# Kernel tuning notes

Hardware: AMD Instinct MI355X
Metric: run time of the kernel (lower is better)

## Reference

```python
import jax, jax.numpy as jnp
import numpy as np

N_NODES = 50000
N_EDGES = 800000
D_FEAT = 64
UNITS = 128  # concat=True -> each kernel maps D_FEAT -> UNITS//2


def setup_inputs() -> dict:
    key = jax.random.key(0)
    k1, k2, k3, k4, k5 = jax.random.split(key, 5)
    x = jax.random.normal(k1, (N_NODES, D_FEAT), dtype=jnp.float32)
    edge_index = jax.random.randint(k2, (2, N_EDGES), 0, N_NODES, dtype=jnp.int64)
    edge_weight = jax.random.uniform(k3, (N_EDGES,), dtype=jnp.float32)
    glorot = np.sqrt(6.0 / (D_FEAT + UNITS // 2)).astype(np.float32)
    self_kernel = jax.random.uniform(k4, (D_FEAT, UNITS // 2), dtype=jnp.float32, minval=-glorot, maxval=glorot)
    neighbor_kernel = jax.random.uniform(k5, (D_FEAT, UNITS // 2), dtype=jnp.float32, minval=-glorot, maxval=glorot)
    bias = jnp.zeros((UNITS,), dtype=jnp.float32)
    return {"x": x, "edge_index": edge_index, "edge_weight": edge_weight,
            "self_kernel": self_kernel, "neighbor_kernel": neighbor_kernel, "bias": bias}


def reference(x, edge_index, edge_weight, self_kernel, neighbor_kernel, bias):
    num_nodes = x.shape[0]
    row, col = edge_index[0], edge_index[1]  # row: target node, col: source neighbor
    # gather neighbor features and apply edge weights
    neighbor_x = x[col] * edge_weight[:, None]  # [E, D]
    # segment-mean over incoming edges of each target node
    sums = jax.ops.segment_sum(neighbor_x, row, num_segments=num_nodes)  # [N, D]
    counts = jax.ops.segment_sum(jnp.ones_like(edge_weight), row, num_segments=num_nodes)  # [N]
    neighbor_mean = sums / jnp.maximum(counts, 1.0)[:, None]
    # dual projection + concat (concat=True)
    from_self = x @ self_kernel              # [N, UNITS//2]
    from_neigh = neighbor_mean @ neighbor_kernel  # [N, UNITS//2]
    h = jnp.concatenate([from_self, from_neigh], axis=1) + bias
    h = jax.nn.relu(h)
    # normalize=False -> no l2 normalize
    return h
```

## Files before the change

### kernel.cpp

```cpp
#include <hip/hip_runtime.h>


typedef unsigned long long ull;
typedef __attribute__((ext_vector_type(8))) short bf16x8;
typedef __attribute__((ext_vector_type(4))) float f32x4;

constexpr int N_NODES = 50000;
constexpr int N_EDGES = 800000;
constexpr int D = 64;
constexpr int UNITS = 128;
constexpr int NB = (N_NODES + 255) / 256;
constexpr int SC_EPT = 16;
constexpr int SC_THREADS = 256;
constexpr int SC_CHUNK = SC_EPT * SC_THREADS;
constexpr int SC_BLOCKS = (N_EDGES + SC_CHUNK - 1) / SC_CHUNK;
constexpr int NS_EPT = 24;
constexpr int PREP_BLOCKS = 2048;
constexpr int NTILES = N_NODES / 16;
constexpr int PJ_BLOCKS = (NTILES + 3) / 4;

__device__ __forceinline__ unsigned f2bf(float f) {
    unsigned u = __float_as_uint(f);
    return (u + 0x7fffu + ((u >> 16) & 1u)) >> 16;
}
__device__ __forceinline__ float bf2f(unsigned b) {
    return __uint_as_float(b << 16);
}

__global__ __launch_bounds__(256) void prep(const float* __restrict__ x,
                                            unsigned* __restrict__ xh,
                                            const int* __restrict__ ei,
                                            int* __restrict__ partial) {
    constexpr int XW = N_NODES * (D / 2);
    for (int i = blockIdx.x * 256 + threadIdx.x; i < XW; i += PREP_BLOCKS * 256) {
        const float2 v = ((const float2*)x)[i];
        xh[i] = f2bf(v.x) | (f2bf(v.y) << 16);
    }
    if (blockIdx.x < SC_BLOCKS) {
        __shared__ int lh[NB];
        for (int i = threadIdx.x; i < NB; i += 256) lh[i] = 0;
        __syncthreads();
        const int base4 = blockIdx.x * (SC_CHUNK / 4);
        #pragma unroll
        for (int j = 0; j < 4; ++j) {
            const int idx4 = base4 + threadIdx.x + j * 256;
            if (idx4 * 4 < N_EDGES) {
                const int4 r4 = ((const int4*)ei)[idx4];
                atomicAdd(&lh[r4.x >> 8], 1);
                atomicAdd(&lh[r4.y >> 8], 1);
                atomicAdd(&lh[r4.z >> 8], 1);
                atomicAdd(&lh[r4.w >> 8], 1);
            }
        }
        __syncthreads();
        int* row = partial + (size_t)blockIdx.x * NB;
        for (int i = threadIdx.x; i < NB; i += 256) row[i] = lh[i];
    }
}

__global__ __launch_bounds__(256) void scan_cols(int* __restrict__ partial,
                                                 int* __restrict__ btot) {
    __shared__ int s[256];
    const int b = blockIdx.x;
    const int t = threadIdx.x;
    const int v = (t < SC_BLOCKS) ? partial[(size_t)t * NB + b] : 0;
    s[t] = v;
    __syncthreads();
    for (int d2 = 1; d2 < 256; d2 <<= 1) {
        int u = (t >= d2) ? s[t - d2] : 0;
        __syncthreads();
        s[t] += u;
        __syncthreads();
    }
    if (t < SC_BLOCKS) partial[(size_t)t * NB + b] = s[t] - v;
    if (t == 255) btot[b] = s[255];
}

__global__ __launch_bounds__(SC_THREADS) void edge_scatter(const int* __restrict__ ei,
                                                           const float* __restrict__ ew,
                                                           const int* __restrict__ partial,
                                                           const int* __restrict__ btot,
                                                           ull* __restrict__ packed) {
    __shared__ int sb[256];
    __shared__ int lbase[NB];
    __shared__ int lcur[NB];
    const int t = threadIdx.x;
    const int bv = (t < NB) ? btot[t] : 0;
    sb[t] = bv;
    __syncthreads();
    for (int d2 = 1; d2 < 256; d2 <<= 1) {
        int u = (t >= d2) ? sb[t - d2] : 0;
        __syncthreads();
        sb[t] += u;
        __syncthreads();
    }
    const int* row = partial + (size_t)blockIdx.x * NB;
    if (t < NB) {
        lbase[t] = (sb[t] - bv) + row[t];
        lcur[t]  = 0;
    }
    __syncthreads();

    const int base4 = blockIdx.x * (SC_CHUNK / 4);
    int4   r4[4];
    int4   c4[4];
    float4 w4[4];
    #pragma unroll
    for (int j = 0; j < 4; ++j) {
        const int idx4 = base4 + t + j * 256;
        if (idx4 * 4 < N_EDGES) {
            r4[j] = ((const int4*)ei)[idx4];
            c4[j] = ((const int4*)(ei + N_EDGES))[idx4];
            w4[j] = ((const float4*)ew)[idx4];
        } else {
            r4[j] = make_int4(-1, -1, -1, -1);
            c4[j] = make_int4(0, 0, 0, 0);
            w4[j] = make_float4(0.f, 0.f, 0.f, 0.f);
        }
    }
    #pragma unroll
    for (int j = 0; j < 4; ++j) {
        const int   rr[4] = {r4[j].x, r4[j].y, r4[j].z, r4[j].w};
        const int   cc[4] = {c4[j].x, c4[j].y, c4[j].z, c4[j].w};
        const float ww[4] = {w4[j].x, w4[j].y, w4[j].z, w4[j].w};
        #pragma unroll
        for (int k = 0; k < 4; ++k) {
            const int r = rr[k];
            if (r >= 0) {
                const int bb   = r >> 8;
                const int lpos = atomicAdd(&lcur[bb], 1);
                const unsigned hi = (unsigned)cc[k] | ((unsigned)(r & 255) << 16);
                packed[lbase[bb] + lpos] = ((ull)hi << 32) | (ull)(unsigned)__float_as_uint(ww[k]);
            }
        }
    }
}

__global__ __launch_bounds__(256) void node_sort(const int* __restrict__ btot,
                                                 int* __restrict__ offs,
                                                 const ull* __restrict__ packed,
                                                 unsigned* __restrict__ cedges) {
    __shared__ int cur[256];
    __shared__ int sc[256];
    __shared__ int sBase, sEnd;
    const int b = blockIdx.x;
    const int t = threadIdx.x;

    const int bv = (t < NB) ? btot[t] : 0;
    sc[t] = bv;
    __syncthreads();
    for (int d2 = 1; d2 < 256; d2 <<= 1) {
        int u = (t >= d2) ? sc[t - d2] : 0;
        __syncthreads();
        sc[t] += u;
        __syncthreads();
    }
    if (t == b) { sBase = sc[t] - bv; sEnd = sc[t]; }
    __syncthreads();
    const int s = sBase;
    const int e = sEnd;

    ull st[NS_EPT];
    #pragma unroll
    for (int i = 0; i < NS_EPT; ++i) {
        const int idx = s + t + i * 256;
        st[i] = (idx < e) ? packed[idx] : ~0ull;
    }
    cur[t] = 0;
    __syncthreads();
    #pragma unroll
    for (int i = 0; i < NS_EPT; ++i) {
        if (st[i] != ~0ull) atomicAdd(&cur[(int)((st[i] >> 48) & 0xff)], 1);
    }
    __syncthreads();
    const int v = cur[t];
    sc[t] = v;
    __syncthreads();
    for (int d2 = 1; d2 < 256; d2 <<= 1) {
        int u = (t >= d2) ? sc[t - d2] : 0;
        __syncthreads();
        sc[t] += u;
        __syncthreads();
    }
    const int excl = sc[t] - v;
    const int n = b * 256 + t;
    if (n < N_NODES) offs[n] = s + excl;
    if (b == 0 && t == 0) offs[N_NODES] = N_EDGES;
    cur[t] = excl;
    __syncthreads();
    #pragma unroll
    for (int i = 0; i < NS_EPT; ++i) {
        if (st[i] != ~0ull) {
            const int r8  = (int)((st[i] >> 48) & 0xff);
            const int pos = atomicAdd(&cur[r8], 1);
            const unsigned hi  = (unsigned)(st[i] >> 32);
            const unsigned col = hi & 0xffffu;
            const unsigned wbf = f2bf(__uint_as_float((unsigned)st[i]));
            cedges[s + pos] = (col << 16) | wbf;
        }
    }
}

__global__ __launch_bounds__(256) void sage_aggregate(const unsigned* __restrict__ xh,
                                                      const int* __restrict__ offs,
                                                      const unsigned* __restrict__ cedges,
                                                      unsigned* __restrict__ meanh) {
    const int n = (blockIdx.x * 256 + threadIdx.x) >> 5;
    if (n >= N_NODES) return;
    const int l32 = threadIdx.x & 31;
    const int eg  = l32 >> 3;
    const int wq  = l32 & 7;
    const int s = offs[n];
    const int t = offs[n + 1];

    float ax0 = 0.f, ay0 = 0.f, ax1 = 0.f, ay1 = 0.f;
    float ax2 = 0.f, ay2 = 0.f, ax3 = 0.f, ay3 = 0.f;
    float bx0 = 0.f, by0 = 0.f, bx1 = 0.f, by1 = 0.f;
    float bx2 = 0.f, by2 = 0.f, bx3 = 0.f, by3 = 0.f;

    if (t > s) {
        const int tm1 = t - 1;
        for (int g = s; g < t; g += 8) {
            const int eA = g + eg;
            const int eB = g + 4 + eg;
            const unsigned cA = cedges[min(eA, tm1)];
            const unsigned cB = cedges[min(eB, tm1)];
            const float wA = (eA < t) ? bf2f(cA & 0xffffu) : 0.0f;
            const float wB = (eB < t) ? bf2f(cB & 0xffffu) : 0.0f;
            const uint4 vA = *(const uint4*)(xh + (size_t)(cA >> 16) * (D / 2) + wq * 4);
            const uint4 vB = *(const uint4*)(xh + (size_t)(cB >> 16) * (D / 2) + wq * 4);
            ax0 = fmaf(__uint_as_float(vA.x << 16),         wA, ax0);
            ay0 = fmaf(__uint_as_float(vA.x & 0xffff0000u), wA, ay0);
            ax1 = fmaf(__uint_as_float(vA.y << 16),         wA, ax1);
            ay1 = fmaf(__uint_as_float(vA.y & 0xffff0000u), wA, ay1);
            ax2 = fmaf(__uint_as_float(vA.z << 16),         wA, ax2);
            ay2 = fmaf(__uint_as_float(vA.z & 0xffff0000u), wA, ay2);
            ax3 = fmaf(__uint_as_float(vA.w << 16),         wA, ax3);
            ay3 = fmaf(__uint_as_float(vA.w & 0xffff0000u), wA, ay3);
            bx0 = fmaf(__uint_as_float(vB.x << 16),         wB, bx0);
            by0 = fmaf(__uint_as_float(vB.x & 0xffff0000u), wB, by0);
            bx1 = fmaf(__uint_as_float(vB.y << 16),         wB, bx1);
            by1 = fmaf(__uint_as_float(vB.y & 0xffff0000u), wB, by1);
            bx2 = fmaf(__uint_as_float(vB.z << 16),         wB, bx2);
            by2 = fmaf(__uint_as_float(vB.z & 0xffff0000u), wB, by2);
            bx3 = fmaf(__uint_as_float(vB.w << 16),         wB, bx3);
            by3 = fmaf(__uint_as_float(vB.w & 0xffff0000u), wB, by3);
        }
    }
    float sx0 = ax0 + bx0, sy0 = ay0 + by0;
    float sx1 = ax1 + bx1, sy1 = ay1 + by1;
    float sx2 = ax2 + bx2, sy2 = ay2 + by2;
    float sx3 = ax3 + bx3, sy3 = ay3 + by3;
    sx0 += __shfl_xor(sx0, 8);  sx0 += __shfl_xor(sx0, 16);
    sy0 += __shfl_xor(sy0, 8);  sy0 += __shfl_xor(sy0, 16);
    sx1 += __shfl_xor(sx1, 8);  sx1 += __shfl_xor(sx1, 16);
    sy1 += __shfl_xor(sy1, 8);  sy1 += __shfl_xor(sy1, 16);
    sx2 += __shfl_xor(sx2, 8);  sx2 += __shfl_xor(sx2, 16);
    sy2 += __shfl_xor(sy2, 8);  sy2 += __shfl_xor(sy2, 16);
    sx3 += __shfl_xor(sx3, 8);  sx3 += __shfl_xor(sx3, 16);
    sy3 += __shfl_xor(sy3, 8);  sy3 += __shfl_xor(sy3, 16);

    if (eg == 0) {
        const float inv = 1.0f / fmaxf((float)(t - s), 1.0f);
        uint4 r;
        r.x = f2bf(sx0 * inv) | (f2bf(sy0 * inv) << 16);
        r.y = f2bf(sx1 * inv) | (f2bf(sy1 * inv) << 16);
        r.z = f2bf(sx2 * inv) | (f2bf(sy2 * inv) << 16);
        r.w = f2bf(sx3 * inv) | (f2bf(sy3 * inv) << 16);
        *(uint4*)(meanh + (size_t)n * (D / 2) + wq * 4) = r;
    }
}

__global__ __launch_bounds__(256) void sage_project(const unsigned* __restrict__ xh,
                                                    const unsigned* __restrict__ meanh,
                                                    const float* __restrict__ skern,
                                                    const float* __restrict__ nkern,
                                                    const float* __restrict__ bias,
                                                    float* __restrict__ out) {
    const int lane = threadIdx.x & 63;
    const int wid  = (blockIdx.x * 256 + threadIdx.x) >> 6;
    const int r16  = lane & 15;
    const int g    = lane >> 4;

    bf16x8 bfrag[16];
    #pragma unroll
    for (int ct = 0; ct < 8; ++ct) {
        const float* K = (ct < 4) ? skern : nkern;
        const int col = (ct & 3) * 16 + r16;
        #pragma unroll
        for (int kh = 0; kh < 2; ++kh) {
            bf16x8 f;
            #pragma unroll
            for (int j = 0; j < 8; ++j) {
                const int k = kh * 32 + 8 * g + j;
                f[j] = (short)f2bf(K[k * 64 + col]);
            }
            bfrag[ct * 2 + kh] = f;
        }
    }

    if (wid >= NTILES) return;
    const int n0 = wid * 16;

    const unsigned* xrow = xh    + (size_t)(n0 + r16) * (D / 2);
    const unsigned* mrow = meanh + (size_t)(n0 + r16) * (D / 2);
    const bf16x8 aS0 = *(const bf16x8*)(xrow + 4 * g);
    const bf16x8 aS1 = *(const bf16x8*)(xrow + 16 + 4 * g);
    const bf16x8 aN0 = *(const bf16x8*)(mrow + 4 * g);
    const bf16x8 aN1 = *(const bf16x8*)(mrow + 16 + 4 * g);

    f32x4 acc[8];
    #pragma unroll
    for (int ct = 0; ct < 8; ++ct) {
        f32x4 c = {0.f, 0.f, 0.f, 0.f};
        c = __builtin_amdgcn_mfma_f32_16x16x32_bf16(ct < 4 ? aS0 : aN0, bfrag[ct * 2 + 0], c, 0, 0, 0);
        c = __builtin_amdgcn_mfma_f32_16x16x32_bf16(ct < 4 ? aS1 : aN1, bfrag[ct * 2 + 1], c, 0, 0, 0);
        acc[ct] = c;
    }

    #pragma unroll
    for (int ct = 0; ct < 8; ++ct) {
        const int col = (ct < 4 ? 0 : 64) + (ct & 3) * 16 + r16;
        const float bj = bias[col];
        #pragma unroll
        for (int r = 0; r < 4; ++r) {
            const int node = n0 + 4 * g + r;
            out[(size_t)node * UNITS + col] = fmaxf(acc[ct][r] + bj, 0.0f);
        }
    }
}

extern "C" void kernel_launch(void* const* d_in, const int* in_sizes, int n_in,
                              void* d_out, int out_size, void* d_ws, size_t ws_size,
                              hipStream_t stream) {
    const float* x     = (const float*)d_in[0];
    const int*   ei    = (const int*)  d_in[1];
    const float* ew    = (const float*)d_in[2];
    const float* skern = (const float*)d_in[3];
    const float* nkern = (const float*)d_in[4];
    const float* bias  = (const float*)d_in[5];
    float* out = (float*)d_out;

    auto align256 = [](size_t v) { return (v + 255) & ~size_t(255); };
    const size_t szM  = align256((size_t)SC_BLOCKS * NB * sizeof(int));
    const size_t szT  = align256((size_t)NB * sizeof(int));
    const size_t szNO = align256((size_t)(N_NODES + 1) * sizeof(int));
    const size_t szP  = align256((size_t)N_EDGES * sizeof(ull));
    const size_t szC  = align256((size_t)N_EDGES * sizeof(unsigned));
    const size_t szX  = align256((size_t)N_NODES * (D / 2) * sizeof(unsigned));

    char* w = (char*)d_ws;
    int*      partial = (int*)w;
    int*      btot    = (int*)(w + szM);
    int*      offs    = (int*)(w + szM + szT);
    ull*      packed  = (ull*)(w + szM + szT + szNO);
    unsigned* cedges  = (unsigned*)(w + szM + szT + szNO + szP);
    unsigned* xh      = (unsigned*)(w + szM + szT + szNO + szP + szC);
    unsigned* meanh   = (unsigned*)(w + szM + szT + szNO + szP + szC + szX);
    (void)ws_size; (void)in_sizes; (void)n_in; (void)out_size;

    prep          <<<PREP_BLOCKS, 256, 0, stream>>>(x, xh, ei, partial);
    scan_cols     <<<NB, 256, 0, stream>>>(partial, btot);
    edge_scatter  <<<SC_BLOCKS, SC_THREADS, 0, stream>>>(ei, ew, partial, btot, packed);
    node_sort     <<<NB, SC_THREADS, 0, stream>>>(btot, offs, packed, cedges);
    sage_aggregate<<<(N_NODES * 32 + 255) / 256, 256, 0, stream>>>(xh, offs, cedges, meanh);
    sage_project  <<<PJ_BLOCKS, 256, 0, stream>>>(xh, meanh, skern, nkern, bias, out);
}
```

Measured before the change: 60.52 us.

## Fuse neighbor aggregation and projection into one kernel via shared memory

Merges the aggregate and project kernels into a single 512-thread kernel that handles 16 nodes per block. The bf16 neighbor means go into shared memory instead of a global buffer, and each of the 8 waves computes one 16-column output tile with MFMA. This removes a kernel launch and the global write and read of the mean features. In exchange, every block reloads and converts its weight fragments, and the block-wide barrier makes the projection wait on the slowest node's aggregation.

Measured after the change: 60.44 us, median of 2. No clear change (-0.1%).

```diff
diff --git a/kernel.cpp b/kernel.cpp
--- a/kernel.cpp
+++ b/kernel.cpp
@@ -16,8 +16,7 @@
 constexpr int SC_BLOCKS = (N_EDGES + SC_CHUNK - 1) / SC_CHUNK;
 constexpr int NS_EPT = 24;
 constexpr int PREP_BLOCKS = 2048;
-constexpr int NTILES = N_NODES / 16;
-constexpr int PJ_BLOCKS = (NTILES + 3) / 4;
+constexpr int AP_BLOCKS = N_NODES / 16;
 
 __device__ __forceinline__ unsigned f2bf(float f) {
     unsigned u = __float_as_uint(f);
@@ -201,131 +200,119 @@
     }
 }
 
-__global__ __launch_bounds__(256) void sage_aggregate(const unsigned* __restrict__ xh,
-                                                      const int* __restrict__ offs,
-                                                      const unsigned* __restrict__ cedges,
-                                                      unsigned* __restrict__ meanh) {
-    const int n = (blockIdx.x * 256 + threadIdx.x) >> 5;
-    if (n >= N_NODES) return;
-    const int l32 = threadIdx.x & 31;
-    const int eg  = l32 >> 3;
-    const int wq  = l32 & 7;
-    const int s = offs[n];
-    const int t = offs[n + 1];
-
-    float ax0 = 0.f, ay0 = 0.f, ax1 = 0.f, ay1 = 0.f;
-    float ax2 = 0.f, ay2 = 0.f, ax3 = 0.f, ay3 = 0.f;
-    float bx0 = 0.f, by0 = 0.f, bx1 = 0.f, by1 = 0.f;
-    float bx2 = 0.f, by2 = 0.f, bx3 = 0.f, by3 = 0.f;
-
-    if (t > s) {
-        const int tm1 = t - 1;
-        for (int g = s; g < t; g += 8) {
-            const int eA = g + eg;
-            const int eB = g + 4 + eg;
-            const unsigned cA = cedges[min(eA, tm1)];
-            const unsigned cB = cedges[min(eB, tm1)];
-            const float wA = (eA < t) ? bf2f(cA & 0xffffu) : 0.0f;
-            const float wB = (eB < t) ? bf2f(cB & 0xffffu) : 0.0f;
-            const uint4 vA = *(const uint4*)(xh + (size_t)(cA >> 16) * (D / 2) + wq * 4);
-            const uint4 vB = *(const uint4*)(xh + (size_t)(cB >> 16) * (D / 2) + wq * 4);
-            ax0 = fmaf(__uint_as_float(vA.x << 16),         wA, ax0);
-            ay0 = fmaf(__uint_as_float(vA.x & 0xffff0000u), wA, ay0);
-            ax1 = fmaf(__uint_as_float(vA.y << 16),         wA, ax1);
-            ay1 = fmaf(__uint_as_float(vA.y & 0xffff0000u), wA, ay1);
-            ax2 = fmaf(__uint_as_float(vA.z << 16),         wA, ax2);
-            ay2 = fmaf(__uint_as_float(vA.z & 0xffff0000u), wA, ay2);
-            ax3 = fmaf(__uint_as_float(vA.w << 16),         wA, ax3);
-            ay3 = fmaf(__uint_as_float(vA.w & 0xffff0000u), wA, ay3);
-            bx0 = fmaf(__uint_as_float(vB.x << 16),         wB, bx0);
-            by0 = fmaf(__uint_as_float(vB.x & 0xffff0000u), wB, by0);
-            bx1 = fmaf(__uint_as_float(vB.y << 16),         wB, bx1);
-            by1 = fmaf(__uint_as_float(vB.y & 0xffff0000u), wB, by1);
-            bx2 = fmaf(__uint_as_float(vB.z << 16),         wB, bx2);
-            by2 = fmaf(__uint_as_float(vB.z & 0xffff0000u), wB, by2);
-            bx3 = fmaf(__uint_as_float(vB.w << 16),         wB, bx3);
-            by3 = fmaf(__uint_as_float(vB.w & 0xffff0000u), wB, by3);
-        }
-    }
-    float sx0 = ax0 + bx0, sy0 = ay0 + by0;
-    float sx1 = ax1 + bx1, sy1 = ay1 + by1;
-    float sx2 = ax2 + bx2, sy2 = ay2 + by2;
-    float sx3 = ax3 + bx3, sy3 = ay3 + by3;
-    sx0 += __shfl_xor(sx0, 8);  sx0 += __shfl_xor(sx0, 16);
-    sy0 += __shfl_xor(sy0, 8);  sy0 += __shfl_xor(sy0, 16);
-    sx1 += __shfl_xor(sx1, 8);  sx1 += __shfl_xor(sx1, 16);
-    sy1 += __shfl_xor(sy1, 8);  sy1 += __shfl_xor(sy1, 16);
-    sx2 += __shfl_xor(sx2, 8);  sx2 += __shfl_xor(sx2, 16);
-    sy2 += __shfl_xor(sy2, 8);  sy2 += __shfl_xor(sy2, 16);
-    sx3 += __shfl_xor(sx3, 8);  sx3 += __shfl_xor(sx3, 16);
-    sy3 += __shfl_xor(sy3, 8);  sy3 += __shfl_xor(sy3, 16);
-
-    if (eg == 0) {
-        const float inv = 1.0f / fmaxf((float)(t - s), 1.0f);
-        uint4 r;
-        r.x = f2bf(sx0 * inv) | (f2bf(sy0 * inv) << 16);
-        r.y = f2bf(sx1 * inv) | (f2bf(sy1 * inv) << 16);
-        r.z = f2bf(sx2 * inv) | (f2bf(sy2 * inv) << 16);
-        r.w = f2bf(sx3 * inv) | (f2bf(sy3 * inv) << 16);
-        *(uint4*)(meanh + (size_t)n * (D / 2) + wq * 4) = r;
-    }
-}
-
-__global__ __launch_bounds__(256) void sage_project(const unsigned* __restrict__ xh,
-                                                    const unsigned* __restrict__ meanh,
-                                                    const float* __restrict__ skern,
-                                                    const float* __restrict__ nkern,
-                                                    const float* __restrict__ bias,
-                                                    float* __restrict__ out) {
-    const int lane = threadIdx.x & 63;
-    const int wid  = (blockIdx.x * 256 + threadIdx.x) >> 6;
-    const int r16  = lane & 15;
-    const int g    = lane >> 4;
-
-    bf16x8 bfrag[16];
-    #pragma unroll
-    for (int ct = 0; ct < 8; ++ct) {
-        const float* K = (ct < 4) ? skern : nkern;
-        const int col = (ct & 3) * 16 + r16;
+__global__ __launch_bounds__(512) void sage_agg_proj(const unsigned* __restrict__ xh,
+                                                     const int* __restrict__ offs,
+                                                     const unsigned* __restrict__ cedges,
+                                                     const float* __restrict__ skern,
+                                                     const float* __restrict__ nkern,
+                                                     const float* __restrict__ bias,
+                                                     float* __restrict__ out) {
+    __shared__ unsigned meanl[16][36];
+    const int tid = threadIdx.x;
+    const int n0  = blockIdx.x * 16;
+
+    {
+        const int hw  = tid >> 5;
+        const int l32 = tid & 31;
+        const int eg  = l32 >> 3;
+        const int wq  = l32 & 7;
+        const int n = n0 + hw;
+        const int s = offs[n];
+        const int t = offs[n + 1];
+
+        float ax0 = 0.f, ay0 = 0.f, ax1 = 0.f, ay1 = 0.f;
+        float ax2 = 0.f, ay2 = 0.f, ax3 = 0.f, ay3 = 0.f;
+        float bx0 = 0.f, by0 = 0.f, bx1 = 0.f, by1 = 0.f;
+        float bx2 = 0.f, by2 = 0.f, bx3 = 0.f, by3 = 0.f;
+
+        if (t > s) {
+            const int tm1 = t - 1;
+            for (int g = s; g < t; g += 8) {
+                const int eA = g + eg;
+                const int eB = g + 4 + eg;
+                const unsigned cA = cedges[min(eA, tm1)];
+                const unsigned cB = cedges[min(eB, tm1)];
+                const float wA = (eA < t) ? bf2f(cA & 0xffffu) : 0.0f;
+                const float wB = (eB < t) ? bf2f(cB & 0xffffu) : 0.0f;
+                const uint4 vA = *(const uint4*)(xh + (size_t)(cA >> 16) * (D / 2) + wq * 4);
+                const uint4 vB = *(const uint4*)(xh + (size_t)(cB >> 16) * (D / 2) + wq * 4);
+                ax0 = fmaf(__uint_as_float(vA.x << 16),         wA, ax0);
+                ay0 = fmaf(__uint_as_float(vA.x & 0xffff0000u), wA, ay0);
+                ax1 = fmaf(__uint_as_float(vA.y << 16),         wA, ax1);
+                ay1 = fmaf(__uint_as_float(vA.y & 0xffff0000u), wA, ay1);
+                ax2 = fmaf(__uint_as_float(vA.z << 16),         wA, ax2);
+                ay2 = fmaf(__uint_as_float(vA.z & 0xffff0000u), wA, ay2);
+                ax3 = fmaf(__uint_as_float(vA.w << 16),         wA, ax3);
+                ay3 = fmaf(__uint_as_float(vA.w & 0xffff0000u), wA, ay3);
+                bx0 = fmaf(__uint_as_float(vB.x << 16),         wB, bx0);
+                by0 = fmaf(__uint_as_float(vB.x & 0xffff0000u), wB, by0);
+                bx1 = fmaf(__uint_as_float(vB.y << 16),         wB, bx1);
+                by1 = fmaf(__uint_as_float(vB.y & 0xffff0000u), wB, by1);
+                bx2 = fmaf(__uint_as_float(vB.z << 16),         wB, bx2);
+                by2 = fmaf(__uint_as_float(vB.z & 0xffff0000u), wB, by2);
+                bx3 = fmaf(__uint_as_float(vB.w << 16),         wB, bx3);
+                by3 = fmaf(__uint_as_float(vB.w & 0xffff0000u), wB, by3);
+            }
+        }
+        float sx0 = ax0 + bx0, sy0 = ay0 + by0;
+        float sx1 = ax1 + bx1, sy1 = ay1 + by1;
+        float sx2 = ax2 + bx2, sy2 = ay2 + by2;
+        float sx3 = ax3 + bx3, sy3 = ay3 + by3;
+        sx0 += __shfl_xor(sx0, 8);  sx0 += __shfl_xor(sx0, 16);
+        sy0 += __shfl_xor(sy0, 8);  sy0 += __shfl_xor(sy0, 16);
+        sx1 += __shfl_xor(sx1, 8);  sx1 += __shfl_xor(sx1, 16);
+        sy1 += __shfl_xor(sy1, 8);  sy1 += __shfl_xor(sy1, 16);
+        sx2 += __shfl_xor(sx2, 8);  sx2 += __shfl_xor(sx2, 16);
+        sy2 += __shfl_xor(sy2, 8);  sy2 += __shfl_xor(sy2, 16);
+        sx3 += __shfl_xor(sx3, 8);  sx3 += __shfl_xor(sx3, 16);
+        sy3 += __shfl_xor(sy3, 8);  sy3 += __shfl_xor(sy3, 16);
+
+        if (eg == 0) {
+            const float inv = 1.0f / fmaxf((float)(t - s), 1.0f);
+            uint4 r;
+            r.x = f2bf(sx0 * inv) | (f2bf(sy0 * inv) << 16);
+            r.y = f2bf(sx1 * inv) | (f2bf(sy1 * inv) << 16);
+            r.z = f2bf(sx2 * inv) | (f2bf(sy2 * inv) << 16);
+            r.w = f2bf(sx3 * inv) | (f2bf(sy3 * inv) << 16);
+            *(uint4*)&meanl[hw][wq * 4] = r;
+        }
+    }
+    __syncthreads();
+
+    {
+        const int w    = tid >> 6;
+        const int lane = tid & 63;
+        const int r16  = lane & 15;
+        const int g    = lane >> 4;
+        const float* K = (w < 4) ? skern : nkern;
+        const int col  = (w & 3) * 16 + r16;
+
+        bf16x8 b0, b1;
         #pragma unroll
-        for (int kh = 0; kh < 2; ++kh) {
-            bf16x8 f;
-            #pragma unroll
-            for (int j = 0; j < 8; ++j) {
-                const int k = kh * 32 + 8 * g + j;
-                f[j] = (short)f2bf(K[k * 64 + col]);
-            }
-            bfrag[ct * 2 + kh] = f;
-        }
-    }
-
-    if (wid >= NTILES) return;
-    const int n0 = wid * 16;
-
-    const unsigned* xrow = xh    + (size_t)(n0 + r16) * (D / 2);
-    const unsigned* mrow = meanh + (size_t)(n0 + r16) * (D / 2);
-    const bf16x8 aS0 = *(const bf16x8*)(xrow + 4 * g);
-    const bf16x8 aS1 = *(const bf16x8*)(xrow + 16 + 4 * g);
-    const bf16x8 aN0 = *(const bf16x8*)(mrow + 4 * g);
-    const bf16x8 aN1 = *(const bf16x8*)(mrow + 16 + 4 * g);
-
-    f32x4 acc[8];
-    #pragma unroll
-    for (int ct = 0; ct < 8; ++ct) {
+        for (int j = 0; j < 8; ++j) {
+            b0[j] = (short)f2bf(K[(8 * g + j) * 64 + col]);
+            b1[j] = (short)f2bf(K[(32 + 8 * g + j) * 64 + col]);
+        }
+
+        bf16x8 a0, a1;
+        if (w < 4) {
+            const unsigned* xrow = xh + (size_t)(n0 + r16) * (D / 2);
+            a0 = *(const bf16x8*)(xrow + 4 * g);
+            a1 = *(const bf16x8*)(xrow + 16 + 4 * g);
+        } else {
+            a0 = *(const bf16x8*)&meanl[r16][4 * g];
+            a1 = *(const bf16x8*)&meanl[r16][16 + 4 * g];
+        }
+
         f32x4 c = {0.f, 0.f, 0.f, 0.f};
-        c = __builtin_amdgcn_mfma_f32_16x16x32_bf16(ct < 4 ? aS0 : aN0, bfrag[ct * 2 + 0], c, 0, 0, 0);
-        c = __builtin_amdgcn_mfma_f32_16x16x32_bf16(ct < 4 ? aS1 : aN1, bfrag[ct * 2 + 1], c, 0, 0, 0);
-        acc[ct] = c;
-    }
-
-    #pragma unroll
-    for (int ct = 0; ct < 8; ++ct) {
-        const int col = (ct < 4 ? 0 : 64) + (ct & 3) * 16 + r16;
-        const float bj = bias[col];
+        c = __builtin_amdgcn_mfma_f32_16x16x32_bf16(a0, b0, c, 0, 0, 0);
+        c = __builtin_amdgcn_mfma_f32_16x16x32_bf16(a1, b1, c, 0, 0, 0);
+
+        const int ocol = (w < 4 ? 0 : 64) + (w & 3) * 16 + r16;
+        const float bj = bias[ocol];
         #pragma unroll
         for (int r = 0; r < 4; ++r) {
-            const int node = n0 + 4 * g + r;
-            out[(size_t)node * UNITS + col] = fmaxf(acc[ct][r] + bj, 0.0f);
+            out[(size_t)(n0 + 4 * g + r) * UNITS + ocol] = fmaxf(c[r] + bj, 0.0f);
         }
     }
 }
@@ -347,7 +334,6 @@
     const size_t szNO = align256((size_t)(N_NODES + 1) * sizeof(int));
     const size_t szP  = align256((size_t)N_EDGES * sizeof(ull));
     const size_t szC  = align256((size_t)N_EDGES * sizeof(unsigned));
-    const size_t szX  = align256((size_t)N_NODES * (D / 2) * sizeof(unsigned));
 
     char* w = (char*)d_ws;
     int*      partial = (int*)w;
@@ -356,13 +342,11 @@
     ull*      packed  = (ull*)(w + szM + szT + szNO);
     unsigned* cedges  = (unsigned*)(w + szM + szT + szNO + szP);
     unsigned* xh      = (unsigned*)(w + szM + szT + szNO + szP + szC);
-    unsigned* meanh   = (unsigned*)(w + szM + szT + szNO + szP + szC + szX);
     (void)ws_size; (void)in_sizes; (void)n_in; (void)out_size;
 
-    prep          <<<PREP_BLOCKS, 256, 0, stream>>>(x, xh, ei, partial);
-    scan_cols     <<<NB, 256, 0, stream>>>(partial, btot);
-    edge_scatter  <<<SC_BLOCKS, SC_THREADS, 0, stream>>>(ei, ew, partial, btot, packed);
-    node_sort     <<<NB, SC_THREADS, 0, stream>>>(btot, offs, packed, cedges);
-    sage_aggregate<<<(N_NODES * 32 + 255) / 256, 256, 0, stream>>>(xh, offs, cedges, meanh);
-    sage_project  <<<PJ_BLOCKS, 256, 0, stream>>>(xh, meanh, skern, nkern, bias, out);
-}
+    prep         <<<PREP_BLOCKS, 256, 0, stream>>>(x, xh, ei, partial);
+    scan_cols    <<<NB, 256, 0, stream>>>(partial, btot);
+    edge_scatter <<<SC_BLOCKS, SC_THREADS, 0, stream>>>(ei, ew, partial, btot, packed);
+    node_sort    <<<NB, SC_THREADS, 0, stream>>>(btot, offs, packed, cedges);
+    sage_agg_proj<<<AP_BLOCKS, 512, 0, stream>>>(xh, offs, cedges, skern, nkern, bias, out);
+}
```
